# Performance work log

Measured on AMD Instinct MI355X. Metric: run time of the kernel, lower is better.

The kernel has to match this reference:

```python
import jax, jax.numpy as jnp
import numpy as np

N, D, K, O, DEGREE = 524288, 64, 64, 32, 6


def setup_inputs() -> dict:
    key = jax.random.key(0)
    kz, kT, kC, kb = jax.random.split(key, 4)
    z = jax.random.normal(kz, (N, D), dtype=jnp.float32)
    T = jax.random.normal(kT, (DEGREE, K, D), dtype=jnp.float32)  # T[i-1] == T_i
    C = jax.random.normal(kC, (O, K), dtype=jnp.float32)
    beta = jax.random.normal(kb, (O,), dtype=jnp.float32)
    return {"z": z, "T": T, "C": C, "beta": beta}


def reference(z, T, C, beta):
    degree = T.shape[0]
    k = T.shape[1]
    z = z.reshape(-1, T.shape[2])  # [N, d]
    # P0 = ones(k) (buffer T0), P1 = z @ T1.T (T1 is NOT row-normalized)
    p_prev = jnp.ones((k,), dtype=z.dtype)          # P_{i-2}
    p_curr = jnp.matmul(z, T[0].T)                  # P_{i-1}, [N, k]
    for i in range(2, degree + 1):
        Ti = T[i - 1]
        Ti = Ti / jnp.sum(Ti, axis=1, keepdims=True)  # row-normalize for i >= 2
        coef = (2.0 * i - 1.0) / i
        p_new = jnp.matmul(z, coef * Ti.T) * p_curr - ((i - 1.0) / i) * p_prev
        p_prev, p_curr = p_curr, p_new
    return jnp.matmul(p_curr, C.T) + beta  # [N, o]
```

## Files before the change

### kernel.cpp

```cpp
#include <hip/hip_runtime.h>


typedef _Float16 f16x8 __attribute__((ext_vector_type(8)));
typedef short    s16x8 __attribute__((ext_vector_type(8)));
typedef float    f32x4 __attribute__((ext_vector_type(4)));

#define NN      524288
#define BLOCKS  256
#define THREADS 512
#define NWAVES  8

#define BH_OFF    0
#define CF_OFF    49152
#define SCALE_OFF 53248
#define SCR_OFF   54784
#define SMEM_BYTES (SCR_OFF + NWAVES * 4096)

__device__ __forceinline__ unsigned short f2bf(float x) {
    unsigned u = __builtin_bit_cast(unsigned, x);
    return (unsigned short)((u + 0x7FFFu + ((u >> 16) & 1u)) >> 16);
}

__global__ __launch_bounds__(THREADS) void leg_mfma(
    const float* __restrict__ z, const float* __restrict__ T,
    const float* __restrict__ Cm, const float* __restrict__ beta,
    float* __restrict__ out)
{
    extern __shared__ char smem[];
    float* scale_s = (float*)(smem + SCALE_OFF);
    const int tid  = (int)threadIdx.x;
    const int lane = tid & 63;
    const int wv   = tid >> 6;
    const int lrow = lane & 15;
    const int lhi  = lane >> 4;

    if (tid < 384) {
        const int mat = tid >> 6, kc = tid & 63;
        const float4* tr = (const float4*)(T + (size_t)((mat << 6) + kc) * 64);
        float s = 0.f;
        #pragma unroll
        for (int q = 0; q < 16; ++q) { float4 v = tr[q]; s += v.x + v.y + v.z + v.w; }
        float sc;
        if (mat == 0) sc = 1.f;
        else { const float fi = (float)(mat + 1); sc = (2.f * fi - 1.f) / fi / s; }
        scale_s[tid] = sc;
    }
    __syncthreads();

    for (int g = tid; g < 3072; g += THREADS) {
        const int mat = g >> 9;
        const int s   = (g >> 8) & 1;
        const int f   = (g >> 6) & 3;
        const int l   = g & 63;
        const int kc  = (l & 15) + (f << 4);
        const int d0  = ((l >> 4) << 3) + (s << 5);
        const float sc = scale_s[(mat << 6) + kc];
        const float* src = T + (size_t)((mat << 6) + kc) * 64 + d0;
        const float4 v0 = *(const float4*)(src);
        const float4 v1 = *(const float4*)(src + 4);
        const float vv[8] = {v0.x, v0.y, v0.z, v0.w, v1.x, v1.y, v1.z, v1.w};
        f16x8 hi;
        #pragma unroll
        for (int j = 0; j < 8; ++j) hi[j] = (_Float16)(vv[j] * sc);
        const int fr = (((mat << 1) + s) << 2) + f;
        *(f16x8*)(smem + BH_OFF + fr * 1024 + l * 16) = hi;
    }
    if (tid < 256) {
        const int s  = (tid >> 7) & 1;
        const int fo = (tid >> 6) & 1;
        const int l  = tid & 63;
        const int o  = (l & 15) + (fo << 4);
        const int k0 = ((l >> 4) << 3) + (s << 5);
        const float* src = Cm + (size_t)o * 64 + k0;
        const float4 v0 = *(const float4*)src;
        const float4 v1 = *(const float4*)(src + 4);
        const float vv[8] = {v0.x, v0.y, v0.z, v0.w, v1.x, v1.y, v1.z, v1.w};
        s16x8 fr;
        #pragma unroll
        for (int j = 0; j < 8; ++j) fr[j] = (short)f2bf(vv[j]);
        *(s16x8*)(smem + CF_OFF + ((s << 1) + fo) * 1024 + l * 16) = fr;
    }
    __syncthreads();

    const int    gw      = blockIdx.x * NWAVES + wv;
    const size_t rowbase = (size_t)gw * 256;
    float* scr = (float*)(smem + SCR_OFF + wv * 4096);

    const float beta0 = beta[lrow];
    const float beta1 = beta[16 + lrow];

    f16x8 zh[2][2];

    auto leg_step = [&](int mat, float b, f32x4 (&PC)[2][4], f32x4 (&PT)[2][4]) {
        __builtin_amdgcn_s_setprio(1);
        #pragma unroll
        for (int f = 0; f < 4; ++f) {
            const int fr0 = mat * 8 + f;
            const int fr1 = mat * 8 + 4 + f;
            const f16x8 bh0 = *(const f16x8*)(smem + BH_OFF + fr0 * 1024 + lane * 16);
            const f16x8 bh1 = *(const f16x8*)(smem + BH_OFF + fr1 * 1024 + lane * 16);
            #pragma unroll
            for (int t = 0; t < 2; ++t) {
                f32x4 a = {0.f, 0.f, 0.f, 0.f};
                a = __builtin_amdgcn_mfma_f32_16x16x32_f16(zh[t][0], bh0, a, 0, 0, 0);
                a = __builtin_amdgcn_mfma_f32_16x16x32_f16(zh[t][1], bh1, a, 0, 0, 0);
                #pragma unroll
                for (int r = 0; r < 4; ++r)
                    PT[t][f][r] = a[r] * PC[t][f][r] - b * PT[t][f][r];
            }
        }
        __builtin_amdgcn_s_setprio(0);
    };

    float4 zraw[2][4];
    #pragma unroll
    for (int t = 0; t < 2; ++t)
        #pragma unroll
        for (int s = 0; s < 2; ++s) {
            const float* p = z + (rowbase + t * 16 + lrow) * 64 + (s << 5) + (lhi << 3);
            zraw[t][2 * s]     = *(const float4*)(p);
            zraw[t][2 * s + 1] = *(const float4*)(p + 4);
        }

    for (int it = 0; it < 8; ++it) {
        #pragma unroll
        for (int t = 0; t < 2; ++t)
            #pragma unroll
            for (int s = 0; s < 2; ++s) {
                const float4 q0 = zraw[t][2 * s], q1 = zraw[t][2 * s + 1];
                const float vv[8] = {q0.x, q0.y, q0.z, q0.w, q1.x, q1.y, q1.z, q1.w};
                #pragma unroll
                for (int j = 0; j < 8; ++j) zh[t][s][j] = (_Float16)vv[j];
            }
        if (it < 7) {
            #pragma unroll
            for (int t = 0; t < 2; ++t)
                #pragma unroll
                for (int s = 0; s < 2; ++s) {
                    const float* p = z + (rowbase + (it + 1) * 32 + t * 16 + lrow) * 64
                                       + (s << 5) + (lhi << 3);
                    zraw[t][2 * s]     = *(const float4*)(p);
                    zraw[t][2 * s + 1] = *(const float4*)(p + 4);
                }
        }

        f32x4 pA[2][4], pB[2][4];
        __builtin_amdgcn_s_setprio(1);
        #pragma unroll
        for (int f = 0; f < 4; ++f) {
            const int fr0 = f, fr1 = 4 + f;
            const f16x8 bh0 = *(const f16x8*)(smem + BH_OFF + fr0 * 1024 + lane * 16);
            const f16x8 bh1 = *(const f16x8*)(smem + BH_OFF + fr1 * 1024 + lane * 16);
            #pragma unroll
            for (int t = 0; t < 2; ++t) {
                f32x4 a = {0.f, 0.f, 0.f, 0.f};
                a = __builtin_amdgcn_mfma_f32_16x16x32_f16(zh[t][0], bh0, a, 0, 0, 0);
                a = __builtin_amdgcn_mfma_f32_16x16x32_f16(zh[t][1], bh1, a, 0, 0, 0);
                pA[t][f] = a;
            }
        }
        #pragma unroll
        for (int f = 0; f < 4; ++f) {
            const int fr0 = 8 + f, fr1 = 12 + f;
            const f16x8 bh0 = *(const f16x8*)(smem + BH_OFF + fr0 * 1024 + lane * 16);
            const f16x8 bh1 = *(const f16x8*)(smem + BH_OFF + fr1 * 1024 + lane * 16);
            #pragma unroll
            for (int t = 0; t < 2; ++t) {
                f32x4 a = {0.f, 0.f, 0.f, 0.f};
                a = __builtin_amdgcn_mfma_f32_16x16x32_f16(zh[t][0], bh0, a, 0, 0, 0);
                a = __builtin_amdgcn_mfma_f32_16x16x32_f16(zh[t][1], bh1, a, 0, 0, 0);
                #pragma unroll
                for (int r = 0; r < 4; ++r)
                    pB[t][f][r] = a[r] * pA[t][f][r] - 0.5f;
            }
        }
        __builtin_amdgcn_s_setprio(0);
        leg_step(2, 2.f / 3.f, pB, pA);
        leg_step(3, 3.f / 4.f, pA, pB);
        leg_step(4, 4.f / 5.f, pB, pA);
        leg_step(5, 5.f / 6.f, pA, pB);

        s16x8 ch[2][2];
        #pragma unroll
        for (int s = 0; s < 2; ++s)
            #pragma unroll
            for (int fo = 0; fo < 2; ++fo)
                ch[s][fo] = *(const s16x8*)(smem + CF_OFF + ((s << 1) + fo) * 1024 + lane * 16);
        #pragma unroll
        for (int t = 0; t < 2; ++t) {
            #pragma unroll
            for (int f = 0; f < 4; ++f)
                #pragma unroll
                for (int r = 0; r < 4; ++r) {
                    const int row = lhi * 4 + r;
                    const int k   = (f << 4) + lrow;
                    const int g4  = (k >> 2) ^ row;
                    scr[row * 64 + g4 * 4 + (k & 3)] = pB[t][f][r];
                }
            s16x8 p6h[2];
            #pragma unroll
            for (int s = 0; s < 2; ++s) {
                const int g0 = lhi * 2 + s * 8;
                const float4 q0 = *(const float4*)(scr + lrow * 64 + ((g0)     ^ lrow) * 4);
                const float4 q1 = *(const float4*)(scr + lrow * 64 + ((g0 + 1) ^ lrow) * 4);
                const float vv[8] = {q0.x, q0.y, q0.z, q0.w, q1.x, q1.y, q1.z, q1.w};
                #pragma unroll
                for (int j = 0; j < 8; ++j) p6h[s][j] = (short)f2bf(vv[j]);
            }
            #pragma unroll
            for (int fo = 0; fo < 2; ++fo) {
                f32x4 o = {0.f, 0.f, 0.f, 0.f};
                o = __builtin_amdgcn_mfma_f32_16x16x32_bf16(p6h[0], ch[0][fo], o, 0, 0, 0);
                o = __builtin_amdgcn_mfma_f32_16x16x32_bf16(p6h[1], ch[1][fo], o, 0, 0, 0);
                const float bb = fo ? beta1 : beta0;
                const size_t r0 = rowbase + (size_t)it * 32 + t * 16 + lhi * 4;
                #pragma unroll
                for (int r = 0; r < 4; ++r)
                    out[(r0 + r) * 32 + (fo << 4) + lrow] = o[r] + bb;
            }
        }
    }
}

extern "C" void kernel_launch(void* const* d_in, const int* in_sizes, int n_in,
                              void* d_out, int out_size, void* d_ws, size_t ws_size,
                              hipStream_t stream) {
    const float* z    = (const float*)d_in[0];
    const float* T    = (const float*)d_in[1];
    const float* C    = (const float*)d_in[2];
    const float* beta = (const float*)d_in[3];
    float* out = (float*)d_out;
    (void)in_sizes; (void)n_in; (void)out_size; (void)d_ws; (void)ws_size;

    hipFuncSetAttribute((const void*)leg_mfma,
                        hipFuncAttributeMaxDynamicSharedMemorySize, SMEM_BYTES);
    leg_mfma<<<BLOCKS, THREADS, SMEM_BYTES, stream>>>(z, T, C, beta, out);
}
```

Measured before the change: 51.35 us.

## Double block count, keep C fragments in registers, shrink per-wave scratch

Doubles the grid to 512 blocks, so each wave handles 128 rows over 4 iterations instead of 256 over 8. The C output-projection fragments now load straight from global into registers once per thread, instead of being staged in shared memory and reread each iteration. The per-wave transpose scratch is halved by doing the pB-to-bf16 relayout in two 32-column halves, which cuts LDS to 64KB and may allow more blocks per CU. The cost is more per-block setup (T normalization and conversion done twice as often) and more live registers holding C.

```diff
diff --git a/kernel.cpp b/kernel.cpp
--- a/kernel.cpp
+++ b/kernel.cpp
@@ -6,15 +6,14 @@
 typedef float    f32x4 __attribute__((ext_vector_type(4)));
 
 #define NN      524288
-#define BLOCKS  256
+#define BLOCKS  512
 #define THREADS 512
 #define NWAVES  8
-
-#define BH_OFF    0
-#define CF_OFF    49152
-#define SCALE_OFF 53248
-#define SCR_OFF   54784
-#define SMEM_BYTES (SCR_OFF + NWAVES * 4096)
+#define NITER   4
+
+#define BH_OFF  0
+#define SCR_OFF 49152
+#define SMEM_BYTES 65536
 
 __device__ __forceinline__ unsigned short f2bf(float x) {
     unsigned u = __builtin_bit_cast(unsigned, x);
@@ -27,12 +26,28 @@
     float* __restrict__ out)
 {
     extern __shared__ char smem[];
-    float* scale_s = (float*)(smem + SCALE_OFF);
+    float* scale_s = (float*)(smem + SCR_OFF);
     const int tid  = (int)threadIdx.x;
     const int lane = tid & 63;
     const int wv   = tid >> 6;
     const int lrow = lane & 15;
     const int lhi  = lane >> 4;
+
+    s16x8 ch[2][2];
+    #pragma unroll
+    for (int s = 0; s < 2; ++s)
+        #pragma unroll
+        for (int fo = 0; fo < 2; ++fo) {
+            const int o  = lrow + (fo << 4);
+            const int k0 = (lhi << 3) + (s << 5);
+            const float4 v0 = *(const float4*)(Cm + (size_t)o * 64 + k0);
+            const float4 v1 = *(const float4*)(Cm + (size_t)o * 64 + k0 + 4);
+            const float vv[8] = {v0.x, v0.y, v0.z, v0.w, v1.x, v1.y, v1.z, v1.w};
+            s16x8 fr;
+            #pragma unroll
+            for (int j = 0; j < 8; ++j) fr[j] = (short)f2bf(vv[j]);
+            ch[s][fo] = fr;
+        }
 
     if (tid < 384) {
         const int mat = tid >> 6, kc = tid & 63;
@@ -65,26 +80,11 @@
         const int fr = (((mat << 1) + s) << 2) + f;
         *(f16x8*)(smem + BH_OFF + fr * 1024 + l * 16) = hi;
     }
-    if (tid < 256) {
-        const int s  = (tid >> 7) & 1;
-        const int fo = (tid >> 6) & 1;
-        const int l  = tid & 63;
-        const int o  = (l & 15) + (fo << 4);
-        const int k0 = ((l >> 4) << 3) + (s << 5);
-        const float* src = Cm + (size_t)o * 64 + k0;
-        const float4 v0 = *(const float4*)src;
-        const float4 v1 = *(const float4*)(src + 4);
-        const float vv[8] = {v0.x, v0.y, v0.z, v0.w, v1.x, v1.y, v1.z, v1.w};
-        s16x8 fr;
-        #pragma unroll
-        for (int j = 0; j < 8; ++j) fr[j] = (short)f2bf(vv[j]);
-        *(s16x8*)(smem + CF_OFF + ((s << 1) + fo) * 1024 + l * 16) = fr;
-    }
     __syncthreads();
 
     const int    gw      = blockIdx.x * NWAVES + wv;
-    const size_t rowbase = (size_t)gw * 256;
-    float* scr = (float*)(smem + SCR_OFF + wv * 4096);
+    const size_t rowbase = (size_t)gw * 128;
+    float* scr = (float*)(smem + SCR_OFF) + wv * 512;
 
     const float beta0 = beta[lrow];
     const float beta1 = beta[16 + lrow];
@@ -122,7 +122,7 @@
             zraw[t][2 * s + 1] = *(const float4*)(p + 4);
         }
 
-    for (int it = 0; it < 8; ++it) {
+    for (int it = 0; it < NITER; ++it) {
         #pragma unroll
         for (int t = 0; t < 2; ++t)
             #pragma unroll
@@ -132,7 +132,7 @@
                 #pragma unroll
                 for (int j = 0; j < 8; ++j) zh[t][s][j] = (_Float16)vv[j];
             }
-        if (it < 7) {
+        if (it < NITER - 1) {
             #pragma unroll
             for (int t = 0; t < 2; ++t)
                 #pragma unroll
@@ -180,30 +180,30 @@
         leg_step(4, 4.f / 5.f, pB, pA);
         leg_step(5, 5.f / 6.f, pA, pB);
 
-        s16x8 ch[2][2];
-        #pragma unroll
-        for (int s = 0; s < 2; ++s)
-            #pragma unroll
-            for (int fo = 0; fo < 2; ++fo)
-                ch[s][fo] = *(const s16x8*)(smem + CF_OFF + ((s << 1) + fo) * 1024 + lane * 16);
         #pragma unroll
         for (int t = 0; t < 2; ++t) {
-            #pragma unroll
-            for (int f = 0; f < 4; ++f)
-                #pragma unroll
-                for (int r = 0; r < 4; ++r) {
-                    const int row = lhi * 4 + r;
-                    const int k   = (f << 4) + lrow;
-                    const int g4  = (k >> 2) ^ row;
-                    scr[row * 64 + g4 * 4 + (k & 3)] = pB[t][f][r];
+            s16x8 p6h[2];
+            #pragma unroll
+            for (int s = 0; s < 2; ++s) {
+                #pragma unroll
+                for (int f_ = 0; f_ < 2; ++f_) {
+                    const int f    = 2 * s + f_;
+                    const int colp = (f_ << 4) + lrow;
+                    #pragma unroll
+                    for (int r = 0; r < 4; ++r) {
+                        const int row = lhi * 4 + r;
+                        const int g4  = ((colp >> 2) ^ row) & 7;
+                        scr[row * 32 + g4 * 4 + (colp & 3)] = pB[t][f][r];
+                    }
                 }
-            s16x8 p6h[2];
-            #pragma unroll
-            for (int s = 0; s < 2; ++s) {
-                const int g0 = lhi * 2 + s * 8;
-                const float4 q0 = *(const float4*)(scr + lrow * 64 + ((g0)     ^ lrow) * 4);
-                const float4 q1 = *(const float4*)(scr + lrow * 64 + ((g0 + 1) ^ lrow) * 4);
-                const float vv[8] = {q0.x, q0.y, q0.z, q0.w, q1.x, q1.y, q1.z, q1.w};
+                float vv[8];
+                #pragma unroll
+                for (int jg = 0; jg < 2; ++jg) {
+                    const int g4r = (((lhi << 1) + jg) ^ lrow) & 7;
+                    const float4 q = *(const float4*)(scr + lrow * 32 + g4r * 4);
+                    vv[jg * 4 + 0] = q.x; vv[jg * 4 + 1] = q.y;
+                    vv[jg * 4 + 2] = q.z; vv[jg * 4 + 3] = q.w;
+                }
                 #pragma unroll
                 for (int j = 0; j < 8; ++j) p6h[s][j] = (short)f2bf(vv[j]);
             }
```

Result: slower. 59.96 us (+16.8%).

## Process 64 rows per wave iteration and drop the z register prefetch

Applied to the files above, without the earlier changes.

Each wave iteration now handles two 32-row sub-tiles instead of one, so the loop runs 4 times instead of 8. Each LDS-loaded T fragment is reused across twice as many MFMAs. The software prefetch of the next z tile into registers is removed, and z is loaded and converted at the top of each iteration. This doubles the accumulator register footprint (pA/pB), which risks lower occupancy or spills, and global-load latency is no longer hidden by prefetch.

```diff
diff --git a/kernel.cpp b/kernel.cpp
--- a/kernel.cpp
+++ b/kernel.cpp
@@ -9,6 +9,7 @@
 #define BLOCKS  256
 #define THREADS 512
 #define NWAVES  8
+#define NITER   4
 
 #define BH_OFF    0
 #define CF_OFF    49152
@@ -89,9 +90,10 @@
     const float beta0 = beta[lrow];
     const float beta1 = beta[16 + lrow];
 
-    f16x8 zh[2][2];
-
-    auto leg_step = [&](int mat, float b, f32x4 (&PC)[2][4], f32x4 (&PT)[2][4]) {
+    f16x8 zh[2][2][2];
+
+    auto leg_step = [&](int mat, float b,
+                        f32x4 (&PC)[2][2][4], f32x4 (&PT)[2][2][4]) {
         __builtin_amdgcn_s_setprio(1);
         #pragma unroll
         for (int f = 0; f < 4; ++f) {
@@ -100,51 +102,37 @@
             const f16x8 bh0 = *(const f16x8*)(smem + BH_OFF + fr0 * 1024 + lane * 16);
             const f16x8 bh1 = *(const f16x8*)(smem + BH_OFF + fr1 * 1024 + lane * 16);
             #pragma unroll
-            for (int t = 0; t < 2; ++t) {
-                f32x4 a = {0.f, 0.f, 0.f, 0.f};
-                a = __builtin_amdgcn_mfma_f32_16x16x32_f16(zh[t][0], bh0, a, 0, 0, 0);
-                a = __builtin_amdgcn_mfma_f32_16x16x32_f16(zh[t][1], bh1, a, 0, 0, 0);
-                #pragma unroll
-                for (int r = 0; r < 4; ++r)
-                    PT[t][f][r] = a[r] * PC[t][f][r] - b * PT[t][f][r];
-            }
+            for (int u = 0; u < 2; ++u)
+                #pragma unroll
+                for (int t = 0; t < 2; ++t) {
+                    f32x4 a = {0.f, 0.f, 0.f, 0.f};
+                    a = __builtin_amdgcn_mfma_f32_16x16x32_f16(zh[u][t][0], bh0, a, 0, 0, 0);
+                    a = __builtin_amdgcn_mfma_f32_16x16x32_f16(zh[u][t][1], bh1, a, 0, 0, 0);
+                    #pragma unroll
+                    for (int r = 0; r < 4; ++r)
+                        PT[u][t][f][r] = a[r] * PC[u][t][f][r] - b * PT[u][t][f][r];
+                }
         }
         __builtin_amdgcn_s_setprio(0);
     };
 
-    float4 zraw[2][4];
-    #pragma unroll
-    for (int t = 0; t < 2; ++t)
-        #pragma unroll
-        for (int s = 0; s < 2; ++s) {
-            const float* p = z + (rowbase + t * 16 + lrow) * 64 + (s << 5) + (lhi << 3);
-            zraw[t][2 * s]     = *(const float4*)(p);
-            zraw[t][2 * s + 1] = *(const float4*)(p + 4);
-        }
-
-    for (int it = 0; it < 8; ++it) {
-        #pragma unroll
-        for (int t = 0; t < 2; ++t)
-            #pragma unroll
-            for (int s = 0; s < 2; ++s) {
-                const float4 q0 = zraw[t][2 * s], q1 = zraw[t][2 * s + 1];
-                const float vv[8] = {q0.x, q0.y, q0.z, q0.w, q1.x, q1.y, q1.z, q1.w};
-                #pragma unroll
-                for (int j = 0; j < 8; ++j) zh[t][s][j] = (_Float16)vv[j];
-            }
-        if (it < 7) {
+    for (int it = 0; it < NITER; ++it) {
+        #pragma unroll
+        for (int u = 0; u < 2; ++u)
             #pragma unroll
             for (int t = 0; t < 2; ++t)
                 #pragma unroll
                 for (int s = 0; s < 2; ++s) {
-                    const float* p = z + (rowbase + (it + 1) * 32 + t * 16 + lrow) * 64
+                    const float* p = z + (rowbase + (size_t)it * 64 + u * 32 + t * 16 + lrow) * 64
                                        + (s << 5) + (lhi << 3);
-                    zraw[t][2 * s]     = *(const float4*)(p);
-                    zraw[t][2 * s + 1] = *(const float4*)(p + 4);
-                }
-        }
-
-        f32x4 pA[2][4], pB[2][4];
+                    const float4 q0 = *(const float4*)(p);
+                    const float4 q1 = *(const float4*)(p + 4);
+                    const float vv[8] = {q0.x, q0.y, q0.z, q0.w, q1.x, q1.y, q1.z, q1.w};
+                    #pragma unroll
+                    for (int j = 0; j < 8; ++j) zh[u][t][s][j] = (_Float16)vv[j];
+                }
+
+        f32x4 pA[2][2][4], pB[2][2][4];
         __builtin_amdgcn_s_setprio(1);
         #pragma unroll
         for (int f = 0; f < 4; ++f) {
@@ -152,12 +140,14 @@
             const f16x8 bh0 = *(const f16x8*)(smem + BH_OFF + fr0 * 1024 + lane * 16);
             const f16x8 bh1 = *(const f16x8*)(smem + BH_OFF + fr1 * 1024 + lane * 16);
             #pragma unroll
-            for (int t = 0; t < 2; ++t) {
-                f32x4 a = {0.f, 0.f, 0.f, 0.f};
-                a = __builtin_amdgcn_mfma_f32_16x16x32_f16(zh[t][0], bh0, a, 0, 0, 0);
-                a = __builtin_amdgcn_mfma_f32_16x16x32_f16(zh[t][1], bh1, a, 0, 0, 0);
-                pA[t][f] = a;
-            }
+            for (int u = 0; u < 2; ++u)
+                #pragma unroll
+                for (int t = 0; t < 2; ++t) {
+                    f32x4 a = {0.f, 0.f, 0.f, 0.f};
+                    a = __builtin_amdgcn_mfma_f32_16x16x32_f16(zh[u][t][0], bh0, a, 0, 0, 0);
+                    a = __builtin_amdgcn_mfma_f32_16x16x32_f16(zh[u][t][1], bh1, a, 0, 0, 0);
+                    pA[u][t][f] = a;
+                }
         }
         #pragma unroll
         for (int f = 0; f < 4; ++f) {
@@ -165,14 +155,16 @@
             const f16x8 bh0 = *(const f16x8*)(smem + BH_OFF + fr0 * 1024 + lane * 16);
             const f16x8 bh1 = *(const f16x8*)(smem + BH_OFF + fr1 * 1024 + lane * 16);
             #pragma unroll
-            for (int t = 0; t < 2; ++t) {
-                f32x4 a = {0.f, 0.f, 0.f, 0.f};
-                a = __builtin_amdgcn_mfma_f32_16x16x32_f16(zh[t][0], bh0, a, 0, 0, 0);
-                a = __builtin_amdgcn_mfma_f32_16x16x32_f16(zh[t][1], bh1, a, 0, 0, 0);
-                #pragma unroll
-                for (int r = 0; r < 4; ++r)
-                    pB[t][f][r] = a[r] * pA[t][f][r] - 0.5f;
-            }
+            for (int u = 0; u < 2; ++u)
+                #pragma unroll
+                for (int t = 0; t < 2; ++t) {
+                    f32x4 a = {0.f, 0.f, 0.f, 0.f};
+                    a = __builtin_amdgcn_mfma_f32_16x16x32_f16(zh[u][t][0], bh0, a, 0, 0, 0);
+                    a = __builtin_amdgcn_mfma_f32_16x16x32_f16(zh[u][t][1], bh1, a, 0, 0, 0);
+                    #pragma unroll
+                    for (int r = 0; r < 4; ++r)
+                        pB[u][t][f][r] = a[r] * pA[u][t][f][r] - 0.5f;
+                }
         }
         __builtin_amdgcn_s_setprio(0);
         leg_step(2, 2.f / 3.f, pB, pA);
@@ -187,38 +179,40 @@
             for (int fo = 0; fo < 2; ++fo)
                 ch[s][fo] = *(const s16x8*)(smem + CF_OFF + ((s << 1) + fo) * 1024 + lane * 16);
         #pragma unroll
-        for (int t = 0; t < 2; ++t) {
-            #pragma unroll
-            for (int f = 0; f < 4; ++f)
-                #pragma unroll
-                for (int r = 0; r < 4; ++r) {
-                    const int row = lhi * 4 + r;
-                    const int k   = (f << 4) + lrow;
-                    const int g4  = (k >> 2) ^ row;
-                    scr[row * 64 + g4 * 4 + (k & 3)] = pB[t][f][r];
-                }
-            s16x8 p6h[2];
-            #pragma unroll
-            for (int s = 0; s < 2; ++s) {
-                const int g0 = lhi * 2 + s * 8;
-                const float4 q0 = *(const float4*)(scr + lrow * 64 + ((g0)     ^ lrow) * 4);
-                const float4 q1 = *(const float4*)(scr + lrow * 64 + ((g0 + 1) ^ lrow) * 4);
-                const float vv[8] = {q0.x, q0.y, q0.z, q0.w, q1.x, q1.y, q1.z, q1.w};
-                #pragma unroll
-                for (int j = 0; j < 8; ++j) p6h[s][j] = (short)f2bf(vv[j]);
+        for (int u = 0; u < 2; ++u)
+            #pragma unroll
+            for (int t = 0; t < 2; ++t) {
+                #pragma unroll
+                for (int f = 0; f < 4; ++f)
+                    #pragma unroll
+                    for (int r = 0; r < 4; ++r) {
+                        const int row = lhi * 4 + r;
+                        const int k   = (f << 4) + lrow;
+                        const int g4  = (k >> 2) ^ row;
+                        scr[row * 64 + g4 * 4 + (k & 3)] = pB[u][t][f][r];
+                    }
+                s16x8 p6h[2];
+                #pragma unroll
+                for (int s = 0; s < 2; ++s) {
+                    const int g0 = lhi * 2 + s * 8;
+                    const float4 q0 = *(const float4*)(scr + lrow * 64 + ((g0)     ^ lrow) * 4);
+                    const float4 q1 = *(const float4*)(scr + lrow * 64 + ((g0 + 1) ^ lrow) * 4);
+                    const float vv[8] = {q0.x, q0.y, q0.z, q0.w, q1.x, q1.y, q1.z, q1.w};
+                    #pragma unroll
+                    for (int j = 0; j < 8; ++j) p6h[s][j] = (short)f2bf(vv[j]);
+                }
+                #pragma unroll
+                for (int fo = 0; fo < 2; ++fo) {
+                    f32x4 o = {0.f, 0.f, 0.f, 0.f};
+                    o = __builtin_amdgcn_mfma_f32_16x16x32_bf16(p6h[0], ch[0][fo], o, 0, 0, 0);
+                    o = __builtin_amdgcn_mfma_f32_16x16x32_bf16(p6h[1], ch[1][fo], o, 0, 0, 0);
+                    const float bb = fo ? beta1 : beta0;
+                    const size_t r0 = rowbase + (size_t)it * 64 + u * 32 + t * 16 + lhi * 4;
+                    #pragma unroll
+                    for (int r = 0; r < 4; ++r)
+                        out[(r0 + r) * 32 + (fo << 4) + lrow] = o[r] + bb;
+                }
             }
-            #pragma unroll
-            for (int fo = 0; fo < 2; ++fo) {
-                f32x4 o = {0.f, 0.f, 0.f, 0.f};
-                o = __builtin_amdgcn_mfma_f32_16x16x32_bf16(p6h[0], ch[0][fo], o, 0, 0, 0);
-                o = __builtin_amdgcn_mfma_f32_16x16x32_bf16(p6h[1], ch[1][fo], o, 0, 0, 0);
-                const float bb = fo ? beta1 : beta0;
-                const size_t r0 = rowbase + (size_t)it * 32 + t * 16 + lhi * 4;
-                #pragma unroll
-                for (int r = 0; r < 4; ++r)
-                    out[(r0 + r) * 32 + (fo << 4) + lrow] = o[r] + bb;
-            }
-        }
     }
 }
 
```

After: 51.63 us. Within noise of the previous version (+0.6%).
